# Optimization experiments

Measured on AMD Instinct MI355X. Metric: run time of the kernel, lower is better.

## Reference

```python
import jax, jax.numpy as jnp
import numpy as np

B, N, S, HEADS, D = 8, 512, 64, 16, 256

def setup_inputs() -> dict:
    key = jax.random.key(0)
    ks = jax.random.split(key, 5)
    spatial_pos = jax.random.randint(ks[0], (B, N, S), 0, N)
    H = jax.random.normal(ks[1], (B, N, D), dtype=jnp.float32)
    A = jax.random.uniform(ks[2], (B, N, N), dtype=jnp.float32)
    sigma = jnp.ones((1,), dtype=jnp.float32)
    spatial_emb = jax.random.normal(ks[3], (N, HEADS), dtype=jnp.float32)
    vt_weight = jax.random.normal(ks[4], (1, HEADS), dtype=jnp.float32)
    return {"spatial_pos": spatial_pos, "H": H, "A": A, "sigma": sigma,
            "spatial_emb": spatial_emb, "vt_weight": vt_weight}

def reference(spatial_pos, H, A, sigma, spatial_emb, vt_weight):
    b, n, s = spatial_pos.shape
    heads = spatial_emb.shape[1]
    # padding_idx=0: row 0 of the embedding table is zero
    emb = spatial_emb.at[0].set(0.0)
    spb = emb[spatial_pos]                       # [B, N, S, heads]
    # torch .view reinterprets contiguous memory: reshape, NOT transpose
    spb = spb.reshape(b, heads, n, s)            # [B, heads, N, S]
    spatial_bias = jnp.einsum('bhns,bhms->bhnm', spb, spb)  # [B,heads,N,N]
    # degree-normalized (left) adjacency aggregation
    deg = jnp.sum(A, axis=-1, keepdims=True)     # [B, N, 1]
    nor_A = (deg ** -0.5) * A
    M = jnp.matmul(nor_A, H)                     # [B, N, D]
    # pairwise squared euclidean distance via expansion (same math,
    # avoids materializing [B,N,N,D])
    h2 = jnp.sum(H * H, axis=-1)                 # [B, N]
    m2 = jnp.sum(M * M, axis=-1)                 # [B, N]
    cross = jnp.einsum('bnd,bmd->bnm', H, M)     # [B, N, N]
    d2 = h2[:, :, None] + m2[:, None, :] - 2.0 * cross
    gaussian = jnp.exp(-d2 / (2.0 * sigma[0] ** 2))  # [B, N, N]
    # virtual-token bias (vt_weight) only touches padded row/col 0,
    # which is sliced off before return -> no effect on output.
    return spatial_bias + gaussian[:, None, :, :]  # [B, heads, N, N]
```

## Files before the change

kernel.cpp:

```cpp
#include <hip/hip_runtime.h>
#include <hip/hip_bf16.h>

#define NB 8
#define NN 512
#define NS 64
#define NH 16
#define ND 256

typedef __attribute__((ext_vector_type(8))) short bf16x8;
typedef __attribute__((ext_vector_type(4))) short bf16x4;
typedef __attribute__((ext_vector_type(4))) float f32x4;

__device__ inline float wred(float v) {
#pragma unroll
  for (int m = 32; m; m >>= 1) v += __shfl_xor(v, m, 64);
  return v;
}
__device__ inline float wred16(float v) {
#pragma unroll
  for (int m = 1; m < 16; m <<= 1) v += __shfl_xor(v, m, 64);
  return v;
}
__device__ inline ushort f2bf(float x) {
  __hip_bfloat16 h = __float2bfloat16(x);
  return *(ushort*)&h;
}

__global__ __launch_bounds__(256) void k_prep(const int* __restrict__ pos,
                                              const float* __restrict__ emb,
                                              const float* __restrict__ H,
                                              const float* __restrict__ A,
                                              __hip_bfloat16* __restrict__ spb,
                                              __hip_bfloat16* __restrict__ Ab,
                                              __hip_bfloat16* __restrict__ Hb,
                                              __hip_bfloat16* __restrict__ HT,
                                              float* __restrict__ rdeg,
                                              float* __restrict__ h2) {
  __shared__ ushort T[64][68];
  int blk = blockIdx.x, tid = threadIdx.x;
  int wave = tid >> 6, lane = tid & 63;

  if (blk < 1024) {
    int t = blk * 256 + tid;
    int idx = pos[t];
    __hip_bfloat16* dst = spb + (size_t)t * NH;
    union { bf16x8 v; ushort h[8]; } u0, u1;
    if (idx == 0) {
#pragma unroll
      for (int i = 0; i < 8; ++i) { u0.h[i] = 0; u1.h[i] = 0; }
    } else {
      const float* er = emb + idx * NH;
#pragma unroll
      for (int i = 0; i < 8; ++i) { u0.h[i] = f2bf(er[i]); u1.h[i] = f2bf(er[8 + i]); }
    }
    *(bf16x8*)(void*)dst = u0.v;
    *(bf16x8*)(void*)(dst + 8) = u1.v;
  } else if (blk < 2048) {
    int row = (blk - 1024) * 4 + wave;
    const float* ar = A + (size_t)row * NN;
    float4 v0 = *(const float4*)(ar + lane * 8);
    float4 v1 = *(const float4*)(ar + lane * 8 + 4);
    float s = v0.x + v0.y + v0.z + v0.w + v1.x + v1.y + v1.z + v1.w;
    union { bf16x8 v; ushort h[8]; } u;
    u.h[0] = f2bf(v0.x); u.h[1] = f2bf(v0.y); u.h[2] = f2bf(v0.z); u.h[3] = f2bf(v0.w);
    u.h[4] = f2bf(v1.x); u.h[5] = f2bf(v1.y); u.h[6] = f2bf(v1.z); u.h[7] = f2bf(v1.w);
    *(bf16x8*)(void*)(Ab + (size_t)row * NN + lane * 8) = u.v;
    s = wred(s);
    if (lane == 0) rdeg[row] = rsqrtf(s);
  } else if (blk < 3072) {
    int row = (blk - 2048) * 4 + wave;
    const float* hr = H + (size_t)row * ND;
    float4 v = *(const float4*)(hr + lane * 4);
    float ss = v.x * v.x + v.y * v.y + v.z * v.z + v.w * v.w;
    union { bf16x4 v4; ushort h[4]; } u;
    u.h[0] = f2bf(v.x); u.h[1] = f2bf(v.y); u.h[2] = f2bf(v.z); u.h[3] = f2bf(v.w);
    *(bf16x4*)(void*)(Hb + (size_t)row * ND + lane * 4) = u.v4;
    ss = wred(ss);
    if (lane == 0) h2[row] = ss;
  } else {
    int bi = blk - 3072;
    int b = bi >> 5, r = bi & 31;
    int d0 = (r >> 3) * 64, n0 = (r & 7) * 64;
    int n = tid >> 2, c = (tid & 3) * 16;
    const float* src = H + ((size_t)b * NN + n0 + n) * ND + d0 + c;
#pragma unroll
    for (int q = 0; q < 4; ++q) {
      float4 f = *(const float4*)(src + q * 4);
      T[n][c + q * 4 + 0] = f2bf(f.x);
      T[n][c + q * 4 + 1] = f2bf(f.y);
      T[n][c + q * 4 + 2] = f2bf(f.z);
      T[n][c + q * 4 + 3] = f2bf(f.w);
    }
    __syncthreads();
    int d = tid >> 2, nc = (tid & 3) * 16;
    union { bf16x8 v; ushort h[8]; } o0, o1;
#pragma unroll
    for (int i = 0; i < 8; ++i) { o0.h[i] = T[nc + i][d]; o1.h[i] = T[nc + 8 + i][d]; }
    __hip_bfloat16* dst = HT + ((size_t)b * ND + d0 + d) * NN + n0 + nc;
    *(bf16x8*)(void*)dst = o0.v;
    *(bf16x8*)(void*)(dst + 8) = o1.v;
  }
}

__global__ __launch_bounds__(256) void k_gemmM(const __hip_bfloat16* __restrict__ Ab,
                                               const __hip_bfloat16* __restrict__ HT,
                                               const float* __restrict__ rdeg,
                                               __hip_bfloat16* __restrict__ Mb,
                                               float* __restrict__ m2p) {
  int wave = threadIdx.x >> 6, lane = threadIdx.x & 63;
  int b = blockIdx.x & 7, t = blockIdx.x >> 3;
  int tile = t * 4 + wave;
  int rt = tile >> 3, ct = tile & 7;
  int r0 = rt * 32, c0 = ct * 32;
  int rl = lane & 15, g4 = lane >> 4;
  const __hip_bfloat16* X = Ab + (size_t)b * NN * NN;
  const __hip_bfloat16* Y = HT + (size_t)b * ND * NN;
  f32x4 acc[2][2];
#pragma unroll
  for (int i = 0; i < 2; ++i)
#pragma unroll
    for (int j = 0; j < 2; ++j) { acc[i][j][0] = 0.f; acc[i][j][1] = 0.f; acc[i][j][2] = 0.f; acc[i][j][3] = 0.f; }
#pragma unroll
  for (int kk = 0; kk < NN / 32; ++kk) {
    int kb = kk * 32 + g4 * 8;
    bf16x8 a[2], bv[2];
#pragma unroll
    for (int i = 0; i < 2; ++i)
      a[i] = *(const bf16x8*)(const void*)(X + (size_t)(r0 + i * 16 + rl) * NN + kb);
#pragma unroll
    for (int j = 0; j < 2; ++j)
      bv[j] = *(const bf16x8*)(const void*)(Y + (size_t)(c0 + j * 16 + rl) * NN + kb);
#pragma unroll
    for (int i = 0; i < 2; ++i)
#pragma unroll
      for (int j = 0; j < 2; ++j)
        acc[i][j] = __builtin_amdgcn_mfma_f32_16x16x32_bf16(a[i], bv[j], acc[i][j], 0, 0, 0);
  }
#pragma unroll
  for (int i = 0; i < 2; ++i)
#pragma unroll
    for (int r = 0; r < 4; ++r) {
      int row = r0 + i * 16 + g4 * 4 + r;
      float rd = rdeg[b * NN + row];
      float ss = 0.f;
#pragma unroll
      for (int j = 0; j < 2; ++j) {
        float m = rd * acc[i][j][r];
        int col = c0 + j * 16 + rl;
        Mb[((size_t)b * NN + row) * ND + col] = __float2bfloat16(m);
        ss += m * m;
      }
      ss = wred16(ss);
      if (rl == 0) m2p[(size_t)ct * (NB * NN) + b * NN + row] = ss;
    }
}

__global__ __launch_bounds__(256) void k_out(const __hip_bfloat16* __restrict__ Hb,
                                             const __hip_bfloat16* __restrict__ Mb,
                                             const __hip_bfloat16* __restrict__ spb,
                                             const float* __restrict__ h2,
                                             const float* __restrict__ m2p,
                                             const float* __restrict__ sigma,
                                             float* __restrict__ out) {
  __shared__ __align__(16) float Gt[64][68];
  __shared__ __align__(16) float Ot[4][16][68];
  __shared__ float h2s[64], m2s[64];
  int b = blockIdx.x & 7;
  int t2 = blockIdx.x >> 3;
  int ct = t2 & 7, rt = (t2 >> 3) & 7, hg = t2 >> 6;
  int r0 = rt * 64, c0 = ct * 64;
  int tid = threadIdx.x;
  int wave = tid >> 6, lane = tid & 63;
  int rl = lane & 15, g4 = lane >> 4;

  if (tid < 64) {
    h2s[tid] = h2[b * NN + r0 + tid];
  } else if (tid < 128) {
    int c = tid - 64;
    float s = 0.f;
#pragma unroll
    for (int p = 0; p < 8; ++p) s += m2p[(size_t)p * (NB * NN) + b * NN + c0 + c];
    m2s[c] = s;
  }
  __syncthreads();

  {
    const __hip_bfloat16* X = Hb + (size_t)b * NN * ND;
    const __hip_bfloat16* Y = Mb + (size_t)b * NN * ND;
    int rw = wave * 16;
    f32x4 acc[4];
#pragma unroll
    for (int j = 0; j < 4; ++j) { acc[j][0] = 0.f; acc[j][1] = 0.f; acc[j][2] = 0.f; acc[j][3] = 0.f; }
#pragma unroll
    for (int kk = 0; kk < ND / 32; ++kk) {
      int kb = kk * 32 + g4 * 8;
      bf16x8 a = *(const bf16x8*)(const void*)(X + (size_t)(r0 + rw + rl) * ND + kb);
#pragma unroll
      for (int j = 0; j < 4; ++j) {
        bf16x8 bv = *(const bf16x8*)(const void*)(Y + (size_t)(c0 + j * 16 + rl) * ND + kb);
        acc[j] = __builtin_amdgcn_mfma_f32_16x16x32_bf16(a, bv, acc[j], 0, 0, 0);
      }
    }
    float sg = sigma[0];
    float inv = 0.5f / (sg * sg);
#pragma unroll
    for (int j = 0; j < 4; ++j)
#pragma unroll
      for (int r = 0; r < 4; ++r) {
        int rowl = rw + g4 * 4 + r;
        int col = j * 16 + rl;
        float d2 = h2s[rowl] + m2s[col] - 2.0f * acc[j][r];
        Gt[rowl][col] = __expf(-d2 * inv);
      }
  }
  __syncthreads();

  float (*Ow)[68] = Ot[wave];
#pragma unroll 1
  for (int hh = 0; hh < 2; ++hh) {
    int h = hg * 8 + wave * 2 + hh;
    const __hip_bfloat16* Xs = spb + ((size_t)b * NH + h) * NN * NS;
    f32x4 acc[4][4];
#pragma unroll
    for (int i = 0; i < 4; ++i)
#pragma unroll
      for (int j = 0; j < 4; ++j) { acc[i][j][0] = 0.f; acc[i][j][1] = 0.f; acc[i][j][2] = 0.f; acc[i][j][3] = 0.f; }
#pragma unroll
    for (int kk = 0; kk < NS / 32; ++kk) {
      int kb = kk * 32 + g4 * 8;
      bf16x8 a[4], bv[4];
#pragma unroll
      for (int i = 0; i < 4; ++i)
        a[i] = *(const bf16x8*)(const void*)(Xs + (size_t)(r0 + i * 16 + rl) * NS + kb);
#pragma unroll
      for (int j = 0; j < 4; ++j)
        bv[j] = *(const bf16x8*)(const void*)(Xs + (size_t)(c0 + j * 16 + rl) * NS + kb);
#pragma unroll
      for (int i = 0; i < 4; ++i)
#pragma unroll
        for (int j = 0; j < 4; ++j)
          acc[i][j] = __builtin_amdgcn_mfma_f32_16x16x32_bf16(a[i], bv[j], acc[i][j], 0, 0, 0);
    }
    float* ob = out + ((size_t)b * NH + h) * NN * NN;
#pragma unroll
    for (int i = 0; i < 4; ++i) {
#pragma unroll
      for (int j = 0; j < 4; ++j)
#pragma unroll
        for (int r = 0; r < 4; ++r)
          Ow[g4 * 4 + r][j * 16 + rl] = acc[i][j][r];
      asm volatile("s_waitcnt lgkmcnt(0)" ::: "memory");
#pragma unroll
      for (int it = 0; it < 4; ++it) {
        int row = it * 4 + g4;
        int col = rl * 4;
        float4 o = *(const float4*)&Ow[row][col];
        float4 g = *(const float4*)&Gt[i * 16 + row][col];
        float4 w;
        w.x = g.x + o.x; w.y = g.y + o.y; w.z = g.z + o.z; w.w = g.w + o.w;
        *(float4*)&ob[(size_t)(r0 + i * 16 + row) * NN + c0 + col] = w;
      }
      asm volatile("" ::: "memory");
    }
  }
}

extern "C" void kernel_launch(void* const* d_in, const int* in_sizes, int n_in,
                              void* d_out, int out_size, void* d_ws, size_t ws_size,
                              hipStream_t stream) {
  const int* pos = (const int*)d_in[0];
  const float* H = (const float*)d_in[1];
  const float* A = (const float*)d_in[2];
  const float* sigma = (const float*)d_in[3];
  const float* emb = (const float*)d_in[4];
  float* out = (float*)d_out;

  char* ws = (char*)d_ws;
  size_t off = 0;
  auto alloc = [&](size_t bytes) -> void* {
    void* p = ws + off;
    off = (off + bytes + 255) & ~(size_t)255;
    return p;
  };
  __hip_bfloat16* spb = (__hip_bfloat16*)alloc((size_t)NB * NH * NN * NS * 2);
  __hip_bfloat16* Ab  = (__hip_bfloat16*)alloc((size_t)NB * NN * NN * 2);
  __hip_bfloat16* Hb  = (__hip_bfloat16*)alloc((size_t)NB * NN * ND * 2);
  __hip_bfloat16* HT  = (__hip_bfloat16*)alloc((size_t)NB * ND * NN * 2);
  __hip_bfloat16* Mb  = (__hip_bfloat16*)alloc((size_t)NB * NN * ND * 2);
  float* m2p  = (float*)alloc((size_t)8 * NB * NN * 4);
  float* rdeg = (float*)alloc((size_t)NB * NN * 4);
  float* h2   = (float*)alloc((size_t)NB * NN * 4);

  k_prep<<<3328, 256, 0, stream>>>(pos, emb, H, A, spb, Ab, Hb, HT, rdeg, h2);
  k_gemmM<<<256, 256, 0, stream>>>(Ab, HT, rdeg, Mb, m2p);
  k_out<<<1024, 256, 0, stream>>>(Hb, Mb, spb, h2, m2p, sigma, out);
}
```

Measured before the change: 70.38 us.

## Halve gemmM tile rows and merge head groups into 512-thread out blocks

k_gemmM now gives each wave a 16x32 output tile instead of 32x32 and launches twice as many blocks, to spread the small GEMM across more CUs. k_out now uses 512-thread blocks that cover all 16 heads for a 64x64 tile, so the gaussian cross-term GEMM is computed once per tile rather than once per head group. This removes redundant H·M^T work and duplicate gaussian exponentials. In exchange, block count halves, LDS use per block grows, and gemmM reuses less data per wave.

```diff
diff --git a/kernel.cpp b/kernel.cpp
--- a/kernel.cpp
+++ b/kernel.cpp
@@ -111,51 +111,41 @@
   int b = blockIdx.x & 7, t = blockIdx.x >> 3;
   int tile = t * 4 + wave;
   int rt = tile >> 3, ct = tile & 7;
-  int r0 = rt * 32, c0 = ct * 32;
+  int r0 = rt * 16, c0 = ct * 32;
   int rl = lane & 15, g4 = lane >> 4;
   const __hip_bfloat16* X = Ab + (size_t)b * NN * NN;
   const __hip_bfloat16* Y = HT + (size_t)b * ND * NN;
-  f32x4 acc[2][2];
-#pragma unroll
-  for (int i = 0; i < 2; ++i)
-#pragma unroll
-    for (int j = 0; j < 2; ++j) { acc[i][j][0] = 0.f; acc[i][j][1] = 0.f; acc[i][j][2] = 0.f; acc[i][j][3] = 0.f; }
+  f32x4 acc[2];
+#pragma unroll
+  for (int j = 0; j < 2; ++j) { acc[j][0] = 0.f; acc[j][1] = 0.f; acc[j][2] = 0.f; acc[j][3] = 0.f; }
 #pragma unroll
   for (int kk = 0; kk < NN / 32; ++kk) {
     int kb = kk * 32 + g4 * 8;
-    bf16x8 a[2], bv[2];
-#pragma unroll
-    for (int i = 0; i < 2; ++i)
-      a[i] = *(const bf16x8*)(const void*)(X + (size_t)(r0 + i * 16 + rl) * NN + kb);
-#pragma unroll
-    for (int j = 0; j < 2; ++j)
-      bv[j] = *(const bf16x8*)(const void*)(Y + (size_t)(c0 + j * 16 + rl) * NN + kb);
-#pragma unroll
-    for (int i = 0; i < 2; ++i)
-#pragma unroll
-      for (int j = 0; j < 2; ++j)
-        acc[i][j] = __builtin_amdgcn_mfma_f32_16x16x32_bf16(a[i], bv[j], acc[i][j], 0, 0, 0);
-  }
-#pragma unroll
-  for (int i = 0; i < 2; ++i)
-#pragma unroll
-    for (int r = 0; r < 4; ++r) {
-      int row = r0 + i * 16 + g4 * 4 + r;
-      float rd = rdeg[b * NN + row];
-      float ss = 0.f;
-#pragma unroll
-      for (int j = 0; j < 2; ++j) {
-        float m = rd * acc[i][j][r];
-        int col = c0 + j * 16 + rl;
-        Mb[((size_t)b * NN + row) * ND + col] = __float2bfloat16(m);
-        ss += m * m;
-      }
-      ss = wred16(ss);
-      if (rl == 0) m2p[(size_t)ct * (NB * NN) + b * NN + row] = ss;
-    }
-}
-
-__global__ __launch_bounds__(256) void k_out(const __hip_bfloat16* __restrict__ Hb,
+    bf16x8 a = *(const bf16x8*)(const void*)(X + (size_t)(r0 + rl) * NN + kb);
+#pragma unroll
+    for (int j = 0; j < 2; ++j) {
+      bf16x8 bv = *(const bf16x8*)(const void*)(Y + (size_t)(c0 + j * 16 + rl) * NN + kb);
+      acc[j] = __builtin_amdgcn_mfma_f32_16x16x32_bf16(a, bv, acc[j], 0, 0, 0);
+    }
+  }
+#pragma unroll
+  for (int r = 0; r < 4; ++r) {
+    int row = r0 + g4 * 4 + r;
+    float rd = rdeg[b * NN + row];
+    float ss = 0.f;
+#pragma unroll
+    for (int j = 0; j < 2; ++j) {
+      float m = rd * acc[j][r];
+      int col = c0 + j * 16 + rl;
+      Mb[((size_t)b * NN + row) * ND + col] = __float2bfloat16(m);
+      ss += m * m;
+    }
+    ss = wred16(ss);
+    if (rl == 0) m2p[(size_t)ct * (NB * NN) + b * NN + row] = ss;
+  }
+}
+
+__global__ __launch_bounds__(512) void k_out(const __hip_bfloat16* __restrict__ Hb,
                                              const __hip_bfloat16* __restrict__ Mb,
                                              const __hip_bfloat16* __restrict__ spb,
                                              const float* __restrict__ h2,
@@ -163,11 +153,11 @@
                                              const float* __restrict__ sigma,
                                              float* __restrict__ out) {
   __shared__ __align__(16) float Gt[64][68];
-  __shared__ __align__(16) float Ot[4][16][68];
+  __shared__ __align__(16) float Ot[8][16][68];
   __shared__ float h2s[64], m2s[64];
   int b = blockIdx.x & 7;
   int t2 = blockIdx.x >> 3;
-  int ct = t2 & 7, rt = (t2 >> 3) & 7, hg = t2 >> 6;
+  int ct = t2 & 7, rt = t2 >> 3;
   int r0 = rt * 64, c0 = ct * 64;
   int tid = threadIdx.x;
   int wave = tid >> 6, lane = tid & 63;
@@ -184,7 +174,7 @@
   }
   __syncthreads();
 
-  {
+  if (wave < 4) {
     const __hip_bfloat16* X = Hb + (size_t)b * NN * ND;
     const __hip_bfloat16* Y = Mb + (size_t)b * NN * ND;
     int rw = wave * 16;
@@ -218,7 +208,7 @@
   float (*Ow)[68] = Ot[wave];
 #pragma unroll 1
   for (int hh = 0; hh < 2; ++hh) {
-    int h = hg * 8 + wave * 2 + hh;
+    int h = wave * 2 + hh;
     const __hip_bfloat16* Xs = spb + ((size_t)b * NH + h) * NN * NS;
     f32x4 acc[4][4];
 #pragma unroll
@@ -292,6 +282,6 @@
   float* h2   = (float*)alloc((size_t)NB * NN * 4);
 
   k_prep<<<3328, 256, 0, stream>>>(pos, emb, H, A, spb, Ab, Hb, HT, rdeg, h2);
-  k_gemmM<<<256, 256, 0, stream>>>(Ab, HT, rdeg, Mb, m2p);
-  k_out<<<1024, 256, 0, stream>>>(Hb, Mb, spb, h2, m2p, sigma, out);
-}
+  k_gemmM<<<512, 256, 0, stream>>>(Ab, HT, rdeg, Mb, m2p);
+  k_out<<<512, 512, 0, stream>>>(Hb, Mb, spb, h2, m2p, sigma, out);
+}
```

Measured after the change: 64.14 us. -8.9%, faster.
